# Performance work log

Measured on AMD Instinct MI355X. Metric: run time of the kernel, lower is better.

## Reference

```python
import jax, jax.numpy as jnp
import numpy as np

# Module constants derived from default grid_config
D = 59          # depth bins: (60-1)/1
C_OUT = 64
X, Y, Z = 128, 128, 7
STRIDE = 16
GRID_LB = np.array([-51.2, -51.2, -2.5], dtype=np.float32)
GRID_IV = np.array([0.8, 0.8, 1.0], dtype=np.float32)
D0, DSTEP = 1.0, 1.0

B, N, C_IN, H, W = 4, 6, 256, 16, 44


def _voxel_coords():
    xs, ys, zs = np.meshgrid(np.arange(X), np.arange(Y), np.arange(Z), indexing='ij')
    coords = np.stack([xs, ys, zs], axis=-1).reshape(-1, 3).astype(np.float32)
    coords = coords * GRID_IV + GRID_LB  # [V, 3] ego-frame voxel centers
    return coords


def _camera_rig(rng):
    """Realistic 6-camera rig: yawed cameras looking outward, z_cam = forward."""
    c2e = np.zeros((B, N, 4, 4), dtype=np.float32)
    K = np.zeros((B, N, 3, 3), dtype=np.float32)
    for b in range(B):
        for n in range(N):
            a = 2.0 * np.pi * n / N + 0.02 * rng.standard_normal()
            f = np.array([np.cos(a), np.sin(a), 0.0])           # camera forward (z_cam)
            x_cam = np.array([-np.sin(a), np.cos(a), 0.0])      # camera right
            y_cam = np.array([0.0, 0.0, -1.0])                   # camera down
            R = np.stack([x_cam, y_cam, f], axis=1)              # columns = cam axes in ego
            t = 1.0 * f + np.array([0.0, 0.0, 1.5])
            c2e[b, n, :3, :3] = R
            c2e[b, n, :3, 3] = t
            c2e[b, n, 3, 3] = 1.0
            fl = 400.0 + 5.0 * rng.standard_normal()
            K[b, n] = np.array([[fl, 0.0, 352.0], [0.0, fl, 128.0], [0.0, 0.0, 1.0]])
    return c2e, K


def setup_inputs() -> dict:
    key = jax.random.key(0)
    k1, k2, k3 = jax.random.split(key, 3)
    img_feats = jax.random.normal(k1, (B, N, C_IN, H, W), dtype=jnp.float32)
    c2e, K = _camera_rig(np.random.default_rng(0))
    # depth_net: 1x1 conv in_channels -> D + C_OUT
    w_depth = jax.random.normal(k2, (D + C_OUT, C_IN), dtype=jnp.float32) * (1.0 / np.sqrt(C_IN))
    b_depth = jax.random.normal(k3, (D + C_OUT,), dtype=jnp.float32) * 0.01
    return {
        'img_feats': img_feats,
        'cam2ego': jnp.asarray(c2e),
        'cam_intrinsics': jnp.asarray(K),
        'w_depth': w_depth,
        'b_depth': b_depth,
    }


def reference(img_feats, cam2ego, cam_intrinsics, w_depth, b_depth):
    Bc, Nc, C, Hc, Wc = img_feats.shape
    # 1x1 conv == per-pixel linear
    x = jnp.einsum('bnchw,oc->bnhwo', img_feats, w_depth) + b_depth  # [B,N,H,W,D+C_OUT]
    depth = jax.nn.softmax(x[..., :D], axis=-1)                      # [B,N,H,W,D]
    feat = x[..., D:]                                                # [B,N,H,W,C_OUT]

    vox = jnp.asarray(_voxel_coords())                               # [V,3]
    V = vox.shape[0]
    vox_h = jnp.concatenate([vox, jnp.ones((V, 1), vox.dtype)], axis=1)  # [V,4]

    e2c = jnp.linalg.inv(cam2ego)                                    # [B,N,4,4]
    cam = jnp.einsum('bnij,vj->bnvi', e2c, vox_h)[..., :3]           # [B,N,V,3]
    z = cam[..., 2]
    z_safe = jnp.maximum(z, 0.1)
    norm = cam[..., :2] / z_safe[..., None]
    homo = jnp.concatenate([norm, jnp.ones_like(z[..., None])], axis=-1)  # [B,N,V,3]
    img = jnp.einsum('bnij,bnvj->bnvi', cam_intrinsics, homo)[..., :2]
    fc = img / STRIDE                                                # feature-plane coords

    depth_bin = ((z - D0) / DSTEP).astype(jnp.int32)                 # trunc toward 0, matches .long()
    valid = (
        (fc[..., 0] >= 0) & (fc[..., 0] < Wc)
        & (fc[..., 1] >= 0) & (fc[..., 1] < Hc)
        & (z > 0.5)
        & (depth_bin >= 0) & (depth_bin < D)
    )

    u = jnp.clip(fc[..., 0].astype(jnp.int32), 0, Wc - 1)            # [B,N,V]
    v = jnp.clip(fc[..., 1].astype(jnp.int32), 0, Hc - 1)
    d = jnp.clip(depth_bin, 0, D - 1)
    hw = v * Wc + u

    feat_flat = feat.reshape(Bc, Nc, Hc * Wc, C_OUT)
    sampled_feat = jnp.take_along_axis(feat_flat, hw[..., None], axis=2)   # [B,N,V,C_OUT]
    depth_flat = depth.reshape(Bc, Nc, Hc * Wc * D)
    sampled_depth = jnp.take_along_axis(depth_flat, hw * D + d, axis=2)    # [B,N,V]

    wgt = sampled_depth * valid.astype(sampled_depth.dtype)
    # scatter_add at flat_idx == voxel index (identity) -> masked sum over cameras
    bev = jnp.einsum('bnv,bnvc->bvc', wgt, sampled_feat)             # [B,V,C_OUT]
    bev = bev.reshape(Bc, X, Y, Z, C_OUT).sum(axis=3)                # collapse Z
    bev = bev.transpose(0, 3, 2, 1)                                  # [B,C_OUT,Y,X]
    return bev, depth
```

## Files before the change

kernel.cpp:

```cpp
#include <hip/hip_runtime.h>
#include <math.h>

#define D_BINS 59
#define CO     64
#define CI     256
#define NB     4
#define NC     6
#define H_IMG  16
#define W_IMG  44
#define HW     704
#define NPIX   (NB*NC*HW)
#define XD     128
#define YD     128
#define ZD     7
#define NOUT   123

__device__ void inv_rigid(const float* __restrict__ M, float* __restrict__ o) {
    double a = M[0], b = M[1], c = M[2], t0 = M[3];
    double d = M[4], e = M[5], f = M[6], t1 = M[7];
    double g = M[8], h = M[9], ii = M[10], t2 = M[11];
    double A00 = e*ii - f*h, A01 = c*h - b*ii, A02 = b*f - c*e;
    double A10 = f*g - d*ii, A11 = a*ii - c*g, A12 = c*d - a*f;
    double A20 = d*h - e*g,  A21 = b*g - a*h,  A22 = a*e - b*d;
    double det = a*A00 + b*A10 + c*A20;
    double inv = 1.0 / det;
    double r00 = A00*inv, r01 = A01*inv, r02 = A02*inv;
    double r10 = A10*inv, r11 = A11*inv, r12 = A12*inv;
    double r20 = A20*inv, r21 = A21*inv, r22 = A22*inv;
    o[0] = (float)r00; o[1] = (float)r01; o[2]  = (float)r02;
    o[3] = (float)(-(r00*t0 + r01*t1 + r02*t2));
    o[4] = (float)r10; o[5] = (float)r11; o[6]  = (float)r12;
    o[7] = (float)(-(r10*t0 + r11*t1 + r12*t2));
    o[8] = (float)r20; o[9] = (float)r21; o[10] = (float)r22;
    o[11] = (float)(-(r20*t0 + r21*t1 + r22*t2));
}

__global__ __launch_bounds__(256) void k_pre(
    const float* __restrict__ wd, const float* __restrict__ c2e,
    float* __restrict__ wt, float* __restrict__ e2c) {
    const int o = blockIdx.x;
    const int k = threadIdx.x;
    float v = (o < NOUT) ? wd[(size_t)o * CI + k] : 0.f;
    wt[(size_t)k * 128 + o] = v;
    if (blockIdx.x == 0 && k < NB * NC)
        inv_rigid(c2e + k * 16, e2c + k * 12);
}

__global__ __launch_bounds__(512) void k_head(
    const float* __restrict__ img, const float* __restrict__ wt,
    const float* __restrict__ bd, float* __restrict__ depth_out,
    float* __restrict__ feat_ws) {
    __shared__ float smem[8448 + 64];
    float* A_lds = smem;
    float* S = smem + 8448;

    const int px = threadIdx.x;
    const int tid = threadIdx.y * 64 + threadIdx.x;
    const int o0 = __builtin_amdgcn_readfirstlane(threadIdx.y << 4);
    const int p0 = blockIdx.x * 64;
    const int bn = p0 / HW;
    const int hw0 = p0 % HW;
    const float* imgb = img + (size_t)bn * CI * HW + hw0;

    float acc[16];
#pragma unroll
    for (int j = 0; j < 16; ++j) acc[j] = 0.f;

    for (int kc = 0; kc < 4; ++kc) {
#pragma unroll
        for (int it = 0; it < 2; ++it) {
            int idx = tid + it * 512;
            int r = idx >> 4, c4 = idx & 15;
            float4 v = *(const float4*)(imgb + (size_t)(kc * 64 + r) * HW + c4 * 4);
            *(float4*)(A_lds + r * 64 + c4 * 4) = v;
        }
        __syncthreads();
        const float* wr = wt + (size_t)(kc * 64) * 128 + o0;
#pragma unroll 4
        for (int k = 0; k < 64; ++k) {
            float a = A_lds[k * 64 + px];
            const float* w = wr + k * 128;
#pragma unroll
            for (int j = 0; j < 16; ++j)
                acc[j] = fmaf(a, w[j], acc[j]);
        }
        __syncthreads();
    }

    float* X = smem;
#pragma unroll
    for (int j = 0; j < 16; ++j) {
        int o = o0 + j;
        if (o < NOUT) {
            int col = (o < D_BINS) ? o : o + 5;
            X[px * 132 + col] = acc[j] + bd[o];
        }
    }
    __syncthreads();

#pragma unroll
    for (int it = 0; it < 2; ++it) {
        int g = tid + it * 512;
        int p = g >> 4, m = g & 15;
        float4 v = *(const float4*)(X + p * 132 + 64 + m * 4);
        *(float4*)(feat_ws + (size_t)(p0 + p) * CO + m * 4) = v;
    }

    if (tid < 64) {
        float* row = X + tid * 132;
        float m = row[0];
        for (int o = 1; o < D_BINS; ++o) m = fmaxf(m, row[o]);
        float s = 0.f;
        for (int o = 0; o < D_BINS; ++o) {
            float e = __expf(row[o] - m);
            row[o] = e;
            s += e;
        }
        S[tid] = 1.f / s;
    }
    __syncthreads();

    for (int g = tid; g < 64 * D_BINS; g += 512) {
        int p = g / D_BINS;
        int o = g - p * D_BINS;
        depth_out[(size_t)p0 * D_BINS + g] = X[p * 132 + o] * S[p];
    }
}

__global__ __launch_bounds__(256) void k_splat(
    const float* __restrict__ e2c, const float* __restrict__ Kmat,
    const float* __restrict__ depth_g, const float* __restrict__ feat_ws,
    float* __restrict__ bev) {
    const int tx = threadIdx.x;
    const int cq = threadIdx.y;
    const int x = blockIdx.x * 64 + tx;
    const int y = blockIdx.y;
    const int b = blockIdx.z;
    const float wx = (float)x * 0.8f + (-51.2f);
    const float wy = (float)y * 0.8f + (-51.2f);

    float acc[16];
#pragma unroll
    for (int m = 0; m < 16; ++m) acc[m] = 0.f;

    for (int n = 0; n < NC; ++n) {
        const int bn = b * NC + n;
        const float* E = e2c + bn * 12;
        const float* Km = Kmat + bn * 9;
        const float k00 = Km[0], k01 = Km[1], k02 = Km[2];
        const float k10 = Km[3], k11 = Km[4], k12 = Km[5];
        const float e02 = E[2], e12 = E[6], e22 = E[10];
        const float bx0 = E[0] * wx + E[1] * wy + E[3];
        const float bx1 = E[4] * wx + E[5] * wy + E[7];
        const float bx2 = E[8] * wx + E[9] * wy + E[11];
#pragma unroll
        for (int z = 0; z < ZD; ++z) {
            const float wz = -2.5f + (float)z;
            const float cx = bx0 + e02 * wz;
            const float cy = bx1 + e12 * wz;
            const float cz = bx2 + e22 * wz;
            const float zs = fmaxf(cz, 0.1f);
            const float rz = 1.0f / zs;
            const float xn = cx * rz;
            const float yn = cy * rz;
            const float fu = (k00 * xn + k01 * yn + k02) * 0.0625f;
            const float fv = (k10 * xn + k11 * yn + k12) * 0.0625f;
            const int bin = (int)(cz - 1.0f);
            const bool valid = (fu >= 0.f) & (fu < (float)W_IMG) &
                               (fv >= 0.f) & (fv < (float)H_IMG) &
                               (cz > 0.5f) & (bin >= 0) & (bin < D_BINS);
            if (valid) {
                int u = (int)fu;
                int v = (int)fv;
                int hw = v * W_IMG + u;
                float wgt = depth_g[((size_t)bn * HW + hw) * D_BINS + bin];
                const float4* fp =
                    (const float4*)(feat_ws + ((size_t)bn * HW + hw) * CO + cq * 16);
                float4 f0 = fp[0], f1 = fp[1], f2 = fp[2], f3 = fp[3];
                acc[0]  = fmaf(wgt, f0.x, acc[0]);
                acc[1]  = fmaf(wgt, f0.y, acc[1]);
                acc[2]  = fmaf(wgt, f0.z, acc[2]);
                acc[3]  = fmaf(wgt, f0.w, acc[3]);
                acc[4]  = fmaf(wgt, f1.x, acc[4]);
                acc[5]  = fmaf(wgt, f1.y, acc[5]);
                acc[6]  = fmaf(wgt, f1.z, acc[6]);
                acc[7]  = fmaf(wgt, f1.w, acc[7]);
                acc[8]  = fmaf(wgt, f2.x, acc[8]);
                acc[9]  = fmaf(wgt, f2.y, acc[9]);
                acc[10] = fmaf(wgt, f2.z, acc[10]);
                acc[11] = fmaf(wgt, f2.w, acc[11]);
                acc[12] = fmaf(wgt, f3.x, acc[12]);
                acc[13] = fmaf(wgt, f3.y, acc[13]);
                acc[14] = fmaf(wgt, f3.z, acc[14]);
                acc[15] = fmaf(wgt, f3.w, acc[15]);
            }
        }
    }
    float* ob = bev + (((size_t)b * CO + cq * 16) * YD + y) * XD + x;
#pragma unroll
    for (int m = 0; m < 16; ++m) ob[(size_t)m * YD * XD] = acc[m];
}

extern "C" void kernel_launch(void* const* d_in, const int* in_sizes, int n_in,
                              void* d_out, int out_size, void* d_ws, size_t ws_size,
                              hipStream_t stream) {
    const float* img  = (const float*)d_in[0];
    const float* c2e  = (const float*)d_in[1];
    const float* Kmat = (const float*)d_in[2];
    const float* wd   = (const float*)d_in[3];
    const float* bd   = (const float*)d_in[4];
    float* bev = (float*)d_out;
    float* depth_out = bev + (size_t)NB * CO * YD * XD;
    float* feat_ws = (float*)d_ws;
    float* wt  = feat_ws + (size_t)NPIX * CO;
    float* e2c = wt + 256 * 128;

    k_pre<<<128, 256, 0, stream>>>(wd, c2e, wt, e2c);
    k_head<<<NPIX / 64, dim3(64, 8, 1), 0, stream>>>(img, wt, bd, depth_out, feat_ws);
    k_splat<<<dim3(2, YD, NB), dim3(64, 4, 1), 0, stream>>>(e2c, Kmat, depth_out,
                                                            feat_ws, bev);
}
```

Before: 130.7 us.

## Drop weight-transpose kernel, restructure head GEMM and split splat projection across threads

Removes the k_pre launch: the head kernel now reads the untransposed weights directly, and each k_splat block inverts the camera extrinsics itself. The head kernel is rewritten so each 64-lane block handles 8 pixels, with every lane owning up to two output channels held in registers as packed float2 FMAs. Softmax is done with wave shuffles instead of a serial per-pixel loop. k_splat first spreads the 42 camera/z projections across the four channel-group threads and caches index and weight in LDS, so each projection and depth gather is done once instead of four times. In exchange the head uses many more, much smaller blocks with heavy per-lane weight register use, and its stores to the feature buffer are strided.

```diff
diff --git a/kernel.cpp b/kernel.cpp
--- a/kernel.cpp
+++ b/kernel.cpp
@@ -14,6 +14,10 @@
 #define YD     128
 #define ZD     7
 #define NOUT   123
+#define NS     (NC*ZD)
+#define APAD   260
+
+typedef float v2f __attribute__((ext_vector_type(2)));
 
 __device__ void inv_rigid(const float* __restrict__ M, float* __restrict__ o) {
     double a = M[0], b = M[1], c = M[2], t0 = M[3];
@@ -35,147 +39,157 @@
     o[11] = (float)(-(r20*t0 + r21*t1 + r22*t2));
 }
 
-__global__ __launch_bounds__(256) void k_pre(
-    const float* __restrict__ wd, const float* __restrict__ c2e,
-    float* __restrict__ wt, float* __restrict__ e2c) {
-    const int o = blockIdx.x;
-    const int k = threadIdx.x;
-    float v = (o < NOUT) ? wd[(size_t)o * CI + k] : 0.f;
-    wt[(size_t)k * 128 + o] = v;
-    if (blockIdx.x == 0 && k < NB * NC)
-        inv_rigid(c2e + k * 16, e2c + k * 12);
-}
-
-__global__ __launch_bounds__(512) void k_head(
-    const float* __restrict__ img, const float* __restrict__ wt,
+__global__ __launch_bounds__(64, 2) void k_head(
+    const float* __restrict__ img, const float* __restrict__ wd,
     const float* __restrict__ bd, float* __restrict__ depth_out,
     float* __restrict__ feat_ws) {
-    __shared__ float smem[8448 + 64];
-    float* A_lds = smem;
-    float* S = smem + 8448;
-
-    const int px = threadIdx.x;
-    const int tid = threadIdx.y * 64 + threadIdx.x;
-    const int o0 = __builtin_amdgcn_readfirstlane(threadIdx.y << 4);
-    const int p0 = blockIdx.x * 64;
+    __shared__ float A[8 * APAD];
+
+    const int l  = threadIdx.x;
+    const int p0 = blockIdx.x * 8;
     const int bn = p0 / HW;
-    const int hw0 = p0 % HW;
-    const float* imgb = img + (size_t)bn * CI * HW + hw0;
-
-    float acc[16];
-#pragma unroll
-    for (int j = 0; j < 16; ++j) acc[j] = 0.f;
+    const int hw0 = p0 - bn * HW;
+
+    {
+        const int px = l & 7, ko = l >> 3;
+        const float* gsrc = img + (size_t)bn * CI * HW + hw0 + px;
+        float* ldst = A + px * APAD + ko;
+#pragma unroll 8
+        for (int it = 0; it < 32; ++it)
+            ldst[it * 8] = gsrc[(size_t)(it * 8 + ko) * HW];
+    }
+    __syncthreads();
+
+    const int r1 = (l + 64 < NOUT) ? (l + 64) : (NOUT - 1);
+    const float* w0p = wd + (size_t)l * CI;
+    const float* w1p = wd + (size_t)r1 * CI;
+
+    float accA[8], accB[8];
+#pragma unroll
+    for (int p = 0; p < 8; ++p) { accA[p] = 0.f; accB[p] = 0.f; }
 
     for (int kc = 0; kc < 4; ++kc) {
-#pragma unroll
-        for (int it = 0; it < 2; ++it) {
-            int idx = tid + it * 512;
-            int r = idx >> 4, c4 = idx & 15;
-            float4 v = *(const float4*)(imgb + (size_t)(kc * 64 + r) * HW + c4 * 4);
-            *(float4*)(A_lds + r * 64 + c4 * 4) = v;
-        }
-        __syncthreads();
-        const float* wr = wt + (size_t)(kc * 64) * 128 + o0;
-#pragma unroll 4
-        for (int k = 0; k < 64; ++k) {
-            float a = A_lds[k * 64 + px];
-            const float* w = wr + k * 128;
-#pragma unroll
-            for (int j = 0; j < 16; ++j)
-                acc[j] = fmaf(a, w[j], acc[j]);
-        }
-        __syncthreads();
-    }
-
-    float* X = smem;
-#pragma unroll
-    for (int j = 0; j < 16; ++j) {
-        int o = o0 + j;
-        if (o < NOUT) {
-            int col = (o < D_BINS) ? o : o + 5;
-            X[px * 132 + col] = acc[j] + bd[o];
-        }
-    }
-    __syncthreads();
-
-#pragma unroll
-    for (int it = 0; it < 2; ++it) {
-        int g = tid + it * 512;
-        int p = g >> 4, m = g & 15;
-        float4 v = *(const float4*)(X + p * 132 + 64 + m * 4);
-        *(float4*)(feat_ws + (size_t)(p0 + p) * CO + m * 4) = v;
-    }
-
-    if (tid < 64) {
-        float* row = X + tid * 132;
-        float m = row[0];
-        for (int o = 1; o < D_BINS; ++o) m = fmaxf(m, row[o]);
-        float s = 0.f;
-        for (int o = 0; o < D_BINS; ++o) {
-            float e = __expf(row[o] - m);
-            row[o] = e;
-            s += e;
-        }
-        S[tid] = 1.f / s;
-    }
-    __syncthreads();
-
-    for (int g = tid; g < 64 * D_BINS; g += 512) {
-        int p = g / D_BINS;
-        int o = g - p * D_BINS;
-        depth_out[(size_t)p0 * D_BINS + g] = X[p * 132 + o] * S[p];
+        v2f w0[32], w1[32];
+#pragma unroll
+        for (int q = 0; q < 16; ++q) {
+            float4 t0 = *(const float4*)(w0p + kc * 64 + q * 4);
+            w0[2 * q]     = (v2f){t0.x, t0.y};
+            w0[2 * q + 1] = (v2f){t0.z, t0.w};
+            float4 t1 = *(const float4*)(w1p + kc * 64 + q * 4);
+            w1[2 * q]     = (v2f){t1.x, t1.y};
+            w1[2 * q + 1] = (v2f){t1.z, t1.w};
+        }
+#pragma unroll
+        for (int px = 0; px < 8; ++px) {
+            const float* ap = A + px * APAD + kc * 64;
+            v2f s0 = (v2f)(0.f), s1 = (v2f)(0.f);
+#pragma unroll
+            for (int q = 0; q < 16; ++q) {
+                float4 a4 = *(const float4*)(ap + q * 4);
+                v2f a01 = (v2f){a4.x, a4.y};
+                v2f a23 = (v2f){a4.z, a4.w};
+                s0 = __builtin_elementwise_fma(a01, w0[2 * q], s0);
+                s0 = __builtin_elementwise_fma(a23, w0[2 * q + 1], s0);
+                s1 = __builtin_elementwise_fma(a01, w1[2 * q], s1);
+                s1 = __builtin_elementwise_fma(a23, w1[2 * q + 1], s1);
+            }
+            accA[px] += s0.x + s0.y;
+            accB[px] += s1.x + s1.y;
+        }
+    }
+
+    const float b0 = bd[l];
+    const float b1 = (l + 64 < NOUT) ? bd[l + 64] : 0.f;
+#pragma unroll
+    for (int px = 0; px < 8; ++px) {
+        const float x0 = accA[px] + b0;
+        const float x1 = accB[px] + b1;
+        float mx = (l < D_BINS) ? x0 : -INFINITY;
+#pragma unroll
+        for (int m = 1; m < 64; m <<= 1) mx = fmaxf(mx, __shfl_xor(mx, m));
+        const float e = (l < D_BINS) ? __expf(x0 - mx) : 0.f;
+        float s = e;
+#pragma unroll
+        for (int m = 1; m < 64; m <<= 1) s += __shfl_xor(s, m);
+        const size_t p = p0 + px;
+        if (l < D_BINS) depth_out[p * D_BINS + l] = e / s;
+        float* fb = feat_ws + p * CO;
+        if (l >= D_BINS) fb[l - D_BINS] = x0;
+        if (l + 64 < NOUT) fb[l + 5] = x1;
     }
 }
 
 __global__ __launch_bounds__(256) void k_splat(
-    const float* __restrict__ e2c, const float* __restrict__ Kmat,
+    const float* __restrict__ c2e, const float* __restrict__ Kmat,
     const float* __restrict__ depth_g, const float* __restrict__ feat_ws,
     float* __restrict__ bev) {
+    __shared__ int   hw_s[NS][64];
+    __shared__ float wgt_s[NS][64];
+    __shared__ float E_s[NC][12];
+
     const int tx = threadIdx.x;
     const int cq = threadIdx.y;
     const int x = blockIdx.x * 64 + tx;
     const int y = blockIdx.y;
     const int b = blockIdx.z;
+
+    if (cq == 0 && tx < NC)
+        inv_rigid(c2e + (size_t)(b * NC + tx) * 16, &E_s[tx][0]);
+    __syncthreads();
+
     const float wx = (float)x * 0.8f + (-51.2f);
     const float wy = (float)y * 0.8f + (-51.2f);
 
-    float acc[16];
-#pragma unroll
-    for (int m = 0; m < 16; ++m) acc[m] = 0.f;
-
-    for (int n = 0; n < NC; ++n) {
+    for (int s = cq; s < NS; s += 4) {
+        const int n = s / ZD;
+        const int z = s - n * ZD;
         const int bn = b * NC + n;
-        const float* E = e2c + bn * 12;
+        const float* E = &E_s[n][0];
         const float* Km = Kmat + bn * 9;
-        const float k00 = Km[0], k01 = Km[1], k02 = Km[2];
-        const float k10 = Km[3], k11 = Km[4], k12 = Km[5];
-        const float e02 = E[2], e12 = E[6], e22 = E[10];
         const float bx0 = E[0] * wx + E[1] * wy + E[3];
         const float bx1 = E[4] * wx + E[5] * wy + E[7];
         const float bx2 = E[8] * wx + E[9] * wy + E[11];
+        const float wz = -2.5f + (float)z;
+        const float cx = bx0 + E[2]  * wz;
+        const float cy = bx1 + E[6]  * wz;
+        const float cz = bx2 + E[10] * wz;
+        const float zs = fmaxf(cz, 0.1f);
+        const float rz = 1.0f / zs;
+        const float xn = cx * rz;
+        const float yn = cy * rz;
+        const float fu = (Km[0] * xn + Km[1] * yn + Km[2]) * 0.0625f;
+        const float fv = (Km[3] * xn + Km[4] * yn + Km[5]) * 0.0625f;
+        const int bin = (int)(cz - 1.0f);
+        const bool valid = (fu >= 0.f) & (fu < (float)W_IMG) &
+                           (fv >= 0.f) & (fv < (float)H_IMG) &
+                           (cz > 0.5f) & (bin >= 0) & (bin < D_BINS);
+        int hw = -1;
+        float wgt = 0.f;
+        if (valid) {
+            int u = (int)fu;
+            int v = (int)fv;
+            hw = v * W_IMG + u;
+            wgt = depth_g[((size_t)bn * HW + hw) * D_BINS + bin];
+        }
+        hw_s[s][tx] = hw;
+        wgt_s[s][tx] = wgt;
+    }
+    __syncthreads();
+
+    float acc[16];
+#pragma unroll
+    for (int m = 0; m < 16; ++m) acc[m] = 0.f;
+
+    for (int n = 0; n < NC; ++n) {
+        const int bn = b * NC + n;
+        const float* fbase = feat_ws + (size_t)bn * HW * CO + cq * 16;
 #pragma unroll
         for (int z = 0; z < ZD; ++z) {
-            const float wz = -2.5f + (float)z;
-            const float cx = bx0 + e02 * wz;
-            const float cy = bx1 + e12 * wz;
-            const float cz = bx2 + e22 * wz;
-            const float zs = fmaxf(cz, 0.1f);
-            const float rz = 1.0f / zs;
-            const float xn = cx * rz;
-            const float yn = cy * rz;
-            const float fu = (k00 * xn + k01 * yn + k02) * 0.0625f;
-            const float fv = (k10 * xn + k11 * yn + k12) * 0.0625f;
-            const int bin = (int)(cz - 1.0f);
-            const bool valid = (fu >= 0.f) & (fu < (float)W_IMG) &
-                               (fv >= 0.f) & (fv < (float)H_IMG) &
-                               (cz > 0.5f) & (bin >= 0) & (bin < D_BINS);
-            if (valid) {
-                int u = (int)fu;
-                int v = (int)fv;
-                int hw = v * W_IMG + u;
-                float wgt = depth_g[((size_t)bn * HW + hw) * D_BINS + bin];
-                const float4* fp =
-                    (const float4*)(feat_ws + ((size_t)bn * HW + hw) * CO + cq * 16);
+            const int s = n * ZD + z;
+            const int hw = hw_s[s][tx];
+            if (hw >= 0) {
+                const float wgt = wgt_s[s][tx];
+                const float4* fp = (const float4*)(fbase + (size_t)hw * CO);
                 float4 f0 = fp[0], f1 = fp[1], f2 = fp[2], f3 = fp[3];
                 acc[0]  = fmaf(wgt, f0.x, acc[0]);
                 acc[1]  = fmaf(wgt, f0.y, acc[1]);
@@ -212,11 +226,8 @@
     float* bev = (float*)d_out;
     float* depth_out = bev + (size_t)NB * CO * YD * XD;
     float* feat_ws = (float*)d_ws;
-    float* wt  = feat_ws + (size_t)NPIX * CO;
-    float* e2c = wt + 256 * 128;
-
-    k_pre<<<128, 256, 0, stream>>>(wd, c2e, wt, e2c);
-    k_head<<<NPIX / 64, dim3(64, 8, 1), 0, stream>>>(img, wt, bd, depth_out, feat_ws);
-    k_splat<<<dim3(2, YD, NB), dim3(64, 4, 1), 0, stream>>>(e2c, Kmat, depth_out,
+
+    k_head<<<NPIX / 8, 64, 0, stream>>>(img, wd, bd, depth_out, feat_ws);
+    k_splat<<<dim3(2, YD, NB), dim3(64, 4, 1), 0, stream>>>(c2e, Kmat, depth_out,
                                                             feat_ws, bev);
 }
```

Result: slower. 145.9 us (+11.6%).
